# Kernel optimization log

Measured on AMD Instinct MI355X. Metric: run time of the kernel, lower is better.

## Reference

```python
import jax, jax.numpy as jnp
import numpy as np
from jax.scipy.linalg import cholesky, solve_triangular, cho_solve

N, M, D = 16384, 2048, 8
VAR, LS = 1.0, 0.5      # RBF kernel hyperparameters (same for kernel_f and kernel_g)
JITTER = 1e-6
BATCH_RATE = 1.0
HALF_LOG_2PI = 0.5 * float(np.log(2.0 * np.pi))


def rbf(x1, x2):
    # K[i,j] = VAR * exp(-||x1_i - x2_j||^2 / (2 LS^2))
    d2 = (jnp.sum(x1 * x1, 1)[:, None] + jnp.sum(x2 * x2, 1)[None, :]
          - 2.0 * (x1 @ x2.T))
    return VAR * jnp.exp(-0.5 * d2 / (LS * LS))


def setup_inputs() -> dict:
    key = jax.random.key(0)
    ks = jax.random.split(key, 7)
    x = jax.random.normal(ks[0], (N, D), dtype=jnp.float32)
    y = jax.random.normal(ks[1], (N, 1), dtype=jnp.float32)
    z = 2.0 * jax.random.uniform(ks[2], (M, D), dtype=jnp.float32) - 1.0  # inducing inputs in [-1,1]^D
    q_m_f = 0.5 * jax.random.normal(ks[3], (M, 1), dtype=jnp.float32)
    q_m_g = 0.5 * jax.random.normal(ks[4], (M, 1), dtype=jnp.float32)
    # Cholesky-like params: identity plus small strictly-lower noise -> PD covariance
    q_L_f = jnp.eye(M, dtype=jnp.float32) + 0.01 * jnp.tril(
        jax.random.normal(ks[5], (M, M), dtype=jnp.float32), -1)
    q_L_g = jnp.eye(M, dtype=jnp.float32) + 0.01 * jnp.tril(
        jax.random.normal(ks[6], (M, M), dtype=jnp.float32), -1)
    return {"x": x, "y": y, "z": z, "q_m_f": q_m_f, "q_L_f": q_L_f,
            "q_m_g": q_m_g, "q_L_g": q_L_g}


def _gp_marginals_and_kl(x, z, q_m, q_L_raw):
    """Marginal posterior mean/var at x and KL(q(u)||p(u)) for one sparse GP."""
    L_S = jnp.tril(q_L_raw)                     # [M,M]
    Kuu = rbf(z, z) + JITTER * jnp.eye(M, dtype=x.dtype)
    Lk = cholesky(Kuu, lower=True)
    Kfu = rbf(x, z)                             # [N,M]
    # A = Kfu @ Kuu^{-1}
    A = cho_solve((Lk, True), Kfu.T).T          # [N,M]
    m = (A @ q_m)[:, 0]                         # [N]
    # diag(Kff + A (S - Kuu) A^T) = diag(Kff) + diag(A S A^T) - diag(Kfu A^T)
    S = L_S @ L_S.T
    diag_Kff = jnp.full((x.shape[0],), VAR, dtype=x.dtype)
    v = diag_Kff + jnp.sum((A @ S) * A, axis=1) - jnp.sum(A * Kfu, axis=1)
    # KL(N(q_m, S) || N(0, Kuu))
    alpha = solve_triangular(Lk, q_m, lower=True)       # Kuu^{-1/2} m
    W = solve_triangular(Lk, L_S, lower=True)           # Kuu^{-1/2} L_S
    logdet_K = 2.0 * jnp.sum(jnp.log(jnp.diag(Lk)))
    logdet_S = 2.0 * jnp.sum(jnp.log(jnp.abs(jnp.diag(L_S))))
    kl = 0.5 * (jnp.sum(W * W) + jnp.sum(alpha * alpha)
                - jnp.asarray(M, x.dtype) + logdet_K - logdet_S)
    return m, v, kl


def reference(x, y, z, q_m_f, q_L_f, q_m_g, q_L_g):
    m_f, v_f, kl_f = _gp_marginals_and_kl(x, z, q_m_f, q_L_f)
    m_g, v_g, kl_g = _gp_marginals_and_kl(x, z, q_m_g, q_L_g)
    yv = y[:, 0]
    # HetGaussian variational expectation (Saul et al. 2016):
    # E_q[log N(y | f, exp(g))] per point
    expectation = (-HALF_LOG_2PI - 0.5 * m_g
                   - 0.5 * ((yv - m_f) ** 2 + v_f) * jnp.exp(-m_g + 0.5 * v_g))
    elbo = BATCH_RATE * jnp.sum(expectation) - (kl_f + kl_g)
    return -elbo
```

## Files before the change

### kernel.cpp

```cpp
#include <hip/hip_runtime.h>
#include <math.h>

#define NN 16384
#define MM 2048
#define DD 8
#define NB 32
#define GRIDN 512
#define SZB ((size_t)16777216)

constexpr float HLOG2PI = 0.91893853320467274178f;

using short8  = __attribute__((ext_vector_type(8))) short;
using float4v = __attribute__((ext_vector_type(4))) float;

__device__ __forceinline__ float4v f4zero(){ float4v v; v[0]=0.f; v[1]=0.f; v[2]=0.f; v[3]=0.f; return v; }

__device__ __forceinline__ void bfsplit(float v, short& h, short& lo){
  unsigned b = __float_as_uint(v);
  h = (short)(b >> 16);
  float hf = __uint_as_float(b & 0xFFFF0000u);
  lo = (short)(__float_as_uint(v - hf) >> 16);
}
__device__ __forceinline__ float bf2f(short s){
  return __uint_as_float(((unsigned)(unsigned short)s) << 16);
}
__device__ __forceinline__ float4v mfma3(short8 ah, short8 al, short8 bh, short8 bl, float4v c){
  c = __builtin_amdgcn_mfma_f32_16x16x32_bf16(ah, bh, c, 0, 0, 0);
  c = __builtin_amdgcn_mfma_f32_16x16x32_bf16(ah, bl, c, 0, 0, 0);
  c = __builtin_amdgcn_mfma_f32_16x16x32_bf16(al, bh, c, 0, 0, 0);
  return c;
}

__device__ __forceinline__ void gbar0(int* cnt, int* flag, int& gen){
  __syncthreads();
  if (threadIdx.x == 0){
    ++gen;
    __builtin_amdgcn_fence(__ATOMIC_RELEASE, "agent");
    int old = __hip_atomic_fetch_add(cnt, 1, __ATOMIC_RELAXED, __HIP_MEMORY_SCOPE_AGENT);
    if (old == gen*GRIDN - 1){
      __builtin_amdgcn_fence(__ATOMIC_ACQ_REL, "agent");
      __hip_atomic_store(flag, gen, __ATOMIC_RELAXED, __HIP_MEMORY_SCOPE_AGENT);
    } else {
      while (__hip_atomic_load(flag, __ATOMIC_RELAXED, __HIP_MEMORY_SCOPE_AGENT) < gen)
        __builtin_amdgcn_s_sleep(8);
    }
    __builtin_amdgcn_fence(__ATOMIC_ACQUIRE, "agent");
  }
  __syncthreads();
}

__device__ __forceinline__ void gbar_h(int* bar, int xcc, int myN, int nxcd, int& gen){
  __syncthreads();
  if (threadIdx.x == 0){
    ++gen;
    int* lcnt  = bar + xcc*32;
    int* lflag = bar + 512 + xcc*32;
    int* gcnt  = bar + 1024;
    int* gflag = bar + 1056;
    int old = __hip_atomic_fetch_add(lcnt, 1, __ATOMIC_RELAXED, __HIP_MEMORY_SCOPE_AGENT);
    if (old == gen*myN - 1){
      __builtin_amdgcn_fence(__ATOMIC_RELEASE, "agent");
      int g = __hip_atomic_fetch_add(gcnt, 1, __ATOMIC_RELAXED, __HIP_MEMORY_SCOPE_AGENT);
      if (g == gen*nxcd - 1){
        __hip_atomic_store(gflag, gen, __ATOMIC_RELAXED, __HIP_MEMORY_SCOPE_AGENT);
      } else {
        while (__hip_atomic_load(gflag, __ATOMIC_RELAXED, __HIP_MEMORY_SCOPE_AGENT) < gen)
          __builtin_amdgcn_s_sleep(8);
      }
      __builtin_amdgcn_fence(__ATOMIC_ACQUIRE, "agent");
      __hip_atomic_store(lflag, gen, __ATOMIC_RELAXED, __HIP_MEMORY_SCOPE_AGENT);
    } else {
      while (__hip_atomic_load(lflag, __ATOMIC_RELAXED, __HIP_MEMORY_SCOPE_AGENT) < gen)
        __builtin_amdgcn_s_sleep(8);
      __builtin_amdgcn_fence(__ATOMIC_ACQUIRE, "agent");
    }
  }
  __syncthreads();
}

__device__ __forceinline__ float block_reduce(float v, float* scratch){
  int lane = threadIdx.x & 63;
  int w    = threadIdx.x >> 6;
  #pragma unroll
  for (int off=32; off; off>>=1) v += __shfl_down(v, off, 64);
  __syncthreads();
  if (lane==0) scratch[w] = v;
  __syncthreads();
  float r = 0.f;
  if (threadIdx.x < 4) r = scratch[threadIdx.x];
  if (w==0){ r += __shfl_down(r, 2, 64); r += __shfl_down(r, 1, 64); }
  return r;
}

__device__ __forceinline__ void stage64(float (*S)[68], const float* __restrict__ g, int ld, int t){
  #pragma unroll
  for (int p=t; p<1024; p+=256)
    *(float4*)&S[p>>4][(p&15)*4] = *(const float4*)&g[(size_t)(p>>4)*ld + (p&15)*4];
}
__device__ __forceinline__ void tile_gemm_step(float acc[4][4], const float (*As)[68], const float (*Bs)[68], int tx, int ty){
  for (int k=0;k<64;++k){
    float ar[4], bc4[4];
    #pragma unroll
    for (int u=0;u<4;++u){ ar[u]=As[ty*4+u][k]; bc4[u]=Bs[k][tx*4+u]; }
    #pragma unroll
    for (int u=0;u<4;++u)
      #pragma unroll
      for (int v=0;v<4;++v) acc[u][v] += ar[u]*bc4[v];
  }
}
__device__ __forceinline__ void tile_syrk_step(float acc[4][4], const float (*P)[68], const float (*Q)[68], int tx, int ty){
  for (int k=0;k<64;++k){
    float pr[4], qc[4];
    #pragma unroll
    for (int u=0;u<4;++u){ pr[u]=P[ty*4+u][k]; qc[u]=Q[tx*4+u][k]; }
    #pragma unroll
    for (int u=0;u<4;++u)
      #pragma unroll
      for (int v=0;v<4;++v) acc[u][v] += pr[u]*qc[v];
  }
}

__device__ __forceinline__ void factor64_reg(const float (*S)[68],
    float* __restrict__ lkd, float* __restrict__ sdg_, int d, int t){
  if (t < 64){
    float xr[64];
    #pragma unroll
    for (int c4=0;c4<16;++c4) *(float4*)&xr[c4*4] = *(const float4*)&S[t][c4*4];
    float myrp = 1.f;
    #pragma unroll
    for (int j=0;j<64;++j){
      float ajj = __shfl(xr[j], j, 64);
      float piv = sqrtf(fmaxf(ajj, 1e-20f));
      float rp  = 1.f/piv;
      float val = xr[j]*rp;
      if (t==j){ xr[j] = piv; myrp = rp; }
      else if (t>j) xr[j] = val;
      else val = 0.f;
      #pragma unroll
      for (int c=j+1;c<64;++c){
        float vc = __shfl(val, c, 64);
        if (c<=t) xr[c] -= val*vc;
      }
    }
    #pragma unroll
    for (int c=0;c<64;++c) if (c>t) xr[c] = 0.f;
    #pragma unroll
    for (int c4=0;c4<16;++c4)
      *(float4*)&lkd[d*4096 + t*64 + c4*4] = *(float4*)&xr[c4*4];
    sdg_[d*64 + t] = myrp;
  }
}

__global__ __launch_bounds__(256, 2) void factor_coop(
    const float* __restrict__ z,
    const float* __restrict__ qlf, const float* __restrict__ qlg,
    const float* __restrict__ qmf, const float* __restrict__ qmg,
    float* __restrict__ kuu, float* __restrict__ linv,
    float* __restrict__ wf, float* __restrict__ wg,
    float* __restrict__ af, float* __restrict__ ag,
    float* __restrict__ ptmp, float* __restrict__ lkdiag,
    float* __restrict__ sdg, float* __restrict__ ltri, int* __restrict__ bar)
{
  __shared__ float As[64][68];
  __shared__ float Bs[64][68];
  __shared__ float Cs[64][68];
  __shared__ float sd[64];
  __shared__ int binfo[2];
  const int bid = blockIdx.x, t = threadIdx.x;
  const int tx = t & 15, ty = t >> 4;

  int xcc_r;
  asm volatile("s_getreg_b32 %0, hwreg(HW_REG_XCC_ID)" : "=s"(xcc_r));
  const int xcc = xcc_r & 15;
  if (t == 0)
    __hip_atomic_fetch_add(bar + 1152 + xcc*32, 1, __ATOMIC_RELAXED, __HIP_MEMORY_SCOPE_AGENT);
  int gen0 = 0;
  gbar0(bar + 1088, bar + 1120, gen0);
  if (t == 0){
    int myN = __hip_atomic_load(bar + 1152 + xcc*32, __ATOMIC_RELAXED, __HIP_MEMORY_SCOPE_AGENT);
    int nx = 0;
    for (int i=0;i<16;++i)
      nx += (__hip_atomic_load(bar + 1152 + i*32, __ATOMIC_RELAXED, __HIP_MEMORY_SCOPE_AGENT) > 0);
    binfo[0] = myN; binfo[1] = nx;
  }
  __syncthreads();
  const int myN = binfo[0], nxcd = binfo[1];
  int gen = 0;

  if (bid == 0){
    for (int p=t; p<128; p+=256){ int i=p>>1, h=p&1;
      *(float4*)&As[i][h*4] = *(const float4*)&z[(size_t)i*DD + h*4]; }
    __syncthreads();
    float kv[4][4];
    #pragma unroll
    for (int u=0;u<4;++u)
      #pragma unroll
      for (int v=0;v<4;++v){
        float d2=0.f;
        #pragma unroll
        for (int d=0;d<8;++d){ float df=As[ty*4+u][d]-As[tx*4+v][d]; d2+=df*df; }
        kv[u][v] = __expf(-2.f*d2) + ((ty*4+u)==(tx*4+v) ? 1e-6f : 0.f);
      }
    __syncthreads();
    #pragma unroll
    for (int u=0;u<4;++u)
      #pragma unroll
      for (int v=0;v<4;++v) As[ty*4+u][tx*4+v] = kv[u][v];
    __syncthreads();
    factor64_reg(As, lkdiag, sdg, 0, t);
  } else {
    for (int idx=bid; idx<528; idx+=GRIDN-1){
      int r=0; while ((r+1)*(r+2)/2 <= idx) ++r;
      int c = idx - r*(r+1)/2;
      __syncthreads();
      for (int p=t; p<128; p+=256){ int i=p>>1, h=p&1;
        *(float4*)&As[i][h*4] = *(const float4*)&z[(size_t)(r*64+i)*DD + h*4];
        *(float4*)&Bs[i][h*4] = *(const float4*)&z[(size_t)(c*64+i)*DD + h*4]; }
      __syncthreads();
      #pragma unroll
      for (int u=0;u<4;++u){
        float4 o;
        float* ov = (float*)&o;
        #pragma unroll
        for (int v=0;v<4;++v){
          float d2=0.f;
          #pragma unroll
          for (int d=0;d<8;++d){ float df=As[ty*4+u][d]-Bs[tx*4+v][d]; d2+=df*df; }
          float val = __expf(-2.f*d2);
          if (r*64+ty*4+u == c*64+tx*4+v) val += 1e-6f;
          ov[v] = val;
        }
        *(float4*)&kuu[(size_t)(r*64+ty*4+u)*MM + c*64 + tx*4] = o;
      }
    }
  }
  gbar_h(bar, xcc, myN, nxcd, gen);

  for (int kb=0; kb<31; ++kb){
    int T = NB-1 - kb;
    int ntiles = T*(T+1)/2;
    if (bid < ntiles){
      stage64(Cs, lkdiag + kb*4096, 64, t);
      if (t < 64) sd[t] = sdg[kb*64 + t];
    }
    for (int idx=bid; idx<ntiles; idx+=GRIDN){
      int r=0; while ((r+1)*(r+2)/2 <= idx) ++r;
      int c = idx - r*(r+1)/2;
      int bi = kb+1+r, bc = kb+1+c;
      __syncthreads();
      stage64(As, kuu + (size_t)(bi*64)*MM + kb*64, MM, t);
      if (bc != bi) stage64(Bs, kuu + (size_t)(bc*64)*MM + kb*64, MM, t);
      __syncthreads();
      {
        int w = t>>6, l = t&63;
        if (w==0 || (w==1 && bc!=bi)){
          float (*S)[68] = (w==0)? As : Bs;
          float xr[64];
          #pragma unroll
          for (int c4=0;c4<16;++c4) *(float4*)&xr[c4*4] = *(const float4*)&S[l][c4*4];
          #pragma unroll
          for (int j=0;j<64;++j){
            float xj = xr[j]*sd[j];
            xr[j] = xj;
            #pragma unroll
            for (int cc=j+1;cc<64;++cc) xr[cc] -= xj*Cs[cc][j];
          }
          #pragma unroll
          for (int c4=0;c4<16;++c4) *(float4*)&S[l][c4*4] = *(float4*)&xr[c4*4];
        }
      }
      __syncthreads();
      if (bc == kb+1){
        for (int p=t;p<1024;p+=256)
          *(float4*)&ltri[(size_t)(bi*64+(p>>4))*MM + kb*64 + (p&15)*4] =
              *(float4*)&As[p>>4][(p&15)*4];
      }
      float acc[4][4] = {};
      tile_syrk_step(acc, As, (bc==bi)? As : Bs, tx, ty);
      if (bi==kb+1 && bc==kb+1){
        __syncthreads();
        #pragma unroll
        for (int u=0;u<4;++u)
          #pragma unroll
          for (int v=0;v<4;++v) Bs[ty*4+u][tx*4+v] = acc[u][v];
        __syncthreads();
        for (int p=t;p<1024;p+=256){
          int i=p>>4, c4=p&15;
          float4 kv = *(const float4*)&kuu[(size_t)(bi*64+i)*MM + bi*64 + c4*4];
          float4 bv = *(float4*)&Bs[i][c4*4];
          float4 o; o.x=kv.x-bv.x; o.y=kv.y-bv.y; o.z=kv.z-bv.z; o.w=kv.w-bv.w;
          *(float4*)&As[i][c4*4] = o;
        }
        __syncthreads();
        factor64_reg(As, lkdiag, sdg, kb+1, t);
      } else {
        #pragma unroll
        for (int u=0;u<4;++u){
          float4* dst = (float4*)&kuu[(size_t)(bi*64+ty*4+u)*MM + bc*64 + tx*4];
          float4 o = *dst;
          o.x-=acc[u][0]; o.y-=acc[u][1]; o.z-=acc[u][2]; o.w-=acc[u][3];
          *dst = o;
        }
      }
    }
    gbar_h(bar, xcc, myN, nxcd, gen);
  }

  if (bid < NB){
    stage64(As, lkdiag + bid*4096, 64, t);
    __syncthreads();
    if (t < 64){
      for (int j=0;j<64;++j){
        float s = (j==t)?1.f:0.f;
        for (int k=t;k<j;++k) s -= As[j][k]*Bs[k][t];
        Bs[j][t] = (j>=t)? s/As[j][j] : 0.f;
      }
    }
    __syncthreads();
    for (int p=t;p<1024;p+=256){ int i=p>>4, c4=p&15;
      *(float4*)&linv[(size_t)(bid*64+i)*MM + bid*64 + c4*4] = *(float4*)&Bs[i][c4*4]; }
  }
  gbar_h(bar, xcc, myN, nxcd, gen);

  for (int idx=bid; idx<16; idx+=GRIDN){
    int m = idx;
    __syncthreads();
    stage64(As, ltri + (size_t)((2*m+1)*64)*MM + (2*m)*64, MM, t);
    stage64(Bs, linv + (size_t)((2*m)*64)*MM   + (2*m)*64, MM, t);
    __syncthreads();
    float acc[4][4]={};
    tile_gemm_step(acc, As, Bs, tx, ty);
    __syncthreads();
    #pragma unroll
    for (int u=0;u<4;++u)
      #pragma unroll
      for (int v=0;v<4;++v) Bs[ty*4+u][tx*4+v] = acc[u][v];
    stage64(As, linv + (size_t)((2*m+1)*64)*MM + (2*m+1)*64, MM, t);
    __syncthreads();
    float o[4][4]={};
    tile_gemm_step(o, As, Bs, tx, ty);
    #pragma unroll
    for (int u=0;u<4;++u)
      *(float4*)&linv[(size_t)((2*m+1)*64+ty*4+u)*MM + (2*m)*64 + tx*4] =
          make_float4(-o[u][0],-o[u][1],-o[u][2],-o[u][3]);
  }
  gbar_h(bar, xcc, myN, nxcd, gen);

  for (int m=bid; m<8; m+=GRIDN){
    float* pm = ptmp + (size_t)m*128*128;
    for (int ti=0; ti<2; ++ti)
      for (int tj=0; tj<2; ++tj){
        int rb = m*4 + 2 + ti, cb0 = m*4;
        float acc[4][4]={};
        for (int k=tj; k<2; ++k){
          __syncthreads();
          stage64(As, ltri + (size_t)(rb*64)*MM + (cb0+k)*64, MM, t);
          stage64(Bs, linv + (size_t)((cb0+k)*64)*MM + (cb0+tj)*64, MM, t);
          __syncthreads();
          tile_gemm_step(acc, As, Bs, tx, ty);
        }
        #pragma unroll
        for (int u=0;u<4;++u)
          *(float4*)&pm[(size_t)(ti*64+ty*4+u)*128 + tj*64 + tx*4] =
              make_float4(acc[u][0],acc[u][1],acc[u][2],acc[u][3]);
      }
    for (int ti=0; ti<2; ++ti)
      for (int tj=0; tj<2; ++tj){
        int rb = m*4 + 2 + ti;
        float acc[4][4]={};
        for (int k=0; k<=ti; ++k){
          __syncthreads();
          stage64(As, linv + (size_t)(rb*64)*MM + (m*4+2+k)*64, MM, t);
          stage64(Bs, pm + (size_t)(k*64)*128 + tj*64, 128, t);
          __syncthreads();
          tile_gemm_step(acc, As, Bs, tx, ty);
        }
        #pragma unroll
        for (int u=0;u<4;++u)
          *(float4*)&linv[(size_t)(rb*64+ty*4+u)*MM + (m*4+tj)*64 + tx*4] =
              make_float4(-acc[u][0],-acc[u][1],-acc[u][2],-acc[u][3]);
      }
  }
  gbar_h(bar, xcc, myN, nxcd, gen);

  for (int s=2; s<5; ++s){
    int nb = 1<<s, mc = 16>>s, b = 64<<s;
    float* pmb = ptmp + (s==2 ? 131072 : (s==3 ? 393216 : 917504));
    int tiles = mc*nb*nb;
    for (int idx=bid; idx<tiles; idx+=GRIDN){
      int m = idx/(nb*nb), r2 = idx%(nb*nb);
      int ti = r2/nb, tj = r2%nb;
      int rb = m*2*nb + nb + ti, cb0 = m*2*nb;
      float acc[4][4]={};
      for (int k=tj; k<nb; ++k){
        __syncthreads();
        stage64(As, ltri + (size_t)(rb*64)*MM + (cb0+k)*64, MM, t);
        stage64(Bs, linv + (size_t)((cb0+k)*64)*MM + (cb0+tj)*64, MM, t);
        __syncthreads();
        tile_gemm_step(acc, As, Bs, tx, ty);
      }
      float* pm = pmb + (size_t)m*b*b;
      #pragma unroll
      for (int u=0;u<4;++u)
        *(float4*)&pm[(size_t)(ti*64+ty*4+u)*b + tj*64 + tx*4] =
            make_float4(acc[u][0],acc[u][1],acc[u][2],acc[u][3]);
    }
    gbar_h(bar, xcc, myN, nxcd, gen);
    for (int idx=bid; idx<tiles; idx+=GRIDN){
      int m = idx/(nb*nb), r2 = idx%(nb*nb);
      int ti = r2/nb, tj = r2%nb;
      int rb = m*2*nb + nb + ti;
      const float* pm = pmb + (size_t)m*b*b;
      float acc[4][4]={};
      for (int k=0; k<=ti; ++k){
        __syncthreads();
        stage64(As, linv + (size_t)(rb*64)*MM + (m*2*nb+nb+k)*64, MM, t);
        stage64(Bs, pm + (size_t)(k*64)*b + tj*64, b, t);
        __syncthreads();
        tile_gemm_step(acc, As, Bs, tx, ty);
      }
      #pragma unroll
      for (int u=0;u<4;++u)
        *(float4*)&linv[(size_t)(rb*64+ty*4+u)*MM + (m*2*nb+tj)*64 + tx*4] =
            make_float4(-acc[u][0],-acc[u][1],-acc[u][2],-acc[u][3]);
    }
    gbar_h(bar, xcc, myN, nxcd, gen);
  }

  for (int idx=bid; idx<2*528; idx+=GRIDN){
    int gp = idx/528, rem = idx%528;
    int bi=0; while ((bi+1)*(bi+2)/2 <= rem) ++bi;
    int bj = rem - bi*(bi+1)/2;
    const float* ql = gp ? qlg : qlf;
    float* w        = gp ? wg  : wf;
    float acc[4][4]={};
    for (int bk=bj; bk<=bi; ++bk){
      __syncthreads();
      stage64(As, linv + (size_t)(bi*64)*MM + bk*64, MM, t);
      stage64(Bs, ql   + (size_t)(bk*64)*MM + bj*64, MM, t);
      __syncthreads();
      if (bk==bj){
        for (int p=t;p<4096;p+=256){ int i=p>>6, c=p&63; if (i<c) Bs[i][c]=0.f; }
        __syncthreads();
      }
      tile_gemm_step(acc, As, Bs, tx, ty);
    }
    #pragma unroll
    for (int u=0;u<4;++u)
      *(float4*)&w[(size_t)(bi*64+ty*4+u)*MM + bj*64 + tx*4] =
          make_float4(acc[u][0],acc[u][1],acc[u][2],acc[u][3]);
  }
  {
    int gw = bid*4 + (t>>6), l = t&63;
    for (int job=gw; job<4096; job+=GRIDN*4){
      int gp = job>>11, r = job&2047;
      const float* qm = gp ? qmg : qmf;
      float s=0.f;
      for (int c=l; c<=r; c+=64) s += linv[(size_t)r*MM+c]*qm[c];
      #pragma unroll
      for (int off=32; off; off>>=1) s += __shfl_down(s, off, 64);
      if (l==0) (gp ? ag : af)[r] = s;
    }
  }
}


__global__ __launch_bounds__(256) void zfrag_kernel(const float* __restrict__ z,
    short* __restrict__ zfh, short* __restrict__ zfl, float* __restrict__ zn2){
  int zr = blockIdx.x*256 + threadIdx.x;
  float v[DD]; float s = 0.f;
  #pragma unroll
  for (int d=0; d<DD; ++d){ v[d] = z[zr*DD + d]; s += v[d]*v[d]; }
  zn2[zr] = s;
  size_t base = (size_t)(zr >> 4)*512 + (zr & 15)*32;
  #pragma unroll
  for (int k=0; k<32; ++k){
    short h = 0, lo = 0;
    if (k < DD) bfsplit(v[k], h, lo);
    zfh[base + k] = h; zfl[base + k] = lo;
  }
}

__global__ __launch_bounds__(256) void red_small(const float* __restrict__ lkd,
    const float* __restrict__ qlf, const float* __restrict__ qlg,
    const float* __restrict__ af, const float* __restrict__ ag,
    float* __restrict__ scal){
  __shared__ float scratch[4];
  float ldk=0, ldf=0, ldg=0, a2f=0, a2g=0;
  for (int i=threadIdx.x;i<MM;i+=256){
    int kb = i>>6, r = i&63;
    ldk += __logf(lkd[kb*4096 + r*64 + r]);
    ldf += __logf(fabsf(qlf[(size_t)i*MM+i]));
    ldg += __logf(fabsf(qlg[(size_t)i*MM+i]));
    float v = af[i]; a2f += v*v;
    v = ag[i];       a2g += v*v;
  }
  float r;
  r = block_reduce(ldk, scratch); if (threadIdx.x==0) scal[0] = 2.f*r;
  r = block_reduce(ldf, scratch); if (threadIdx.x==0) scal[1] = 2.f*r;
  r = block_reduce(ldg, scratch); if (threadIdx.x==0) scal[2] = 2.f*r;
  r = block_reduce(a2f, scratch); if (threadIdx.x==0) scal[3] = r;
  r = block_reduce(a2g, scratch); if (threadIdx.x==0) scal[4] = r;
}

__global__ __launch_bounds__(256) void redw_kernel(const float* __restrict__ wf,
    const float* __restrict__ wg, float* __restrict__ scal){
  __shared__ float scratch[4];
  size_t start  = (size_t)blockIdx.x*256 + threadIdx.x;
  size_t stride = (size_t)gridDim.x*256;
  float sf=0, sg=0;
  for (size_t p=start;p<(size_t)MM*MM;p+=stride){
    float v=wf[p]; sf += v*v;
    v=wg[p];       sg += v*v;
  }
  float r = block_reduce(sf, scratch);
  if (threadIdx.x==0) atomicAdd(&scal[5], r);
  r = block_reduce(sg, scratch);
  if (threadIdx.x==0) atomicAdd(&scal[6], r);
}

__global__ void kl_kernel(const float* __restrict__ scal, float* __restrict__ out){
  float klf = 0.5f*(scal[5] + scal[3] - (float)MM + scal[0] - scal[1]);
  float klg = 0.5f*(scal[6] + scal[4] - (float)MM + scal[0] - scal[2]);
  out[0] += klf + klg;
}

__global__ __launch_bounds__(256) void split_rowmajor(const float* __restrict__ src,
    short* __restrict__ dh, short* __restrict__ dl){
  int p = blockIdx.x*256 + threadIdx.x;
  int chunk = p >> 9, wi = p & 511;
  int mo = chunk >> 6, ko = chunk & 63;
  int row = mo*16 + (wi >> 5), col = ko*32 + (wi & 31);
  float v = src[(size_t)row*MM + col];
  short h, lo; bfsplit(v, h, lo);
  dh[p] = h; dl[p] = lo;
}

__global__ __launch_bounds__(256) void split_transpose(const float* __restrict__ src,
    short* __restrict__ dh, short* __restrict__ dl){
  __shared__ float tile[32][33];
  int t = threadIdx.x;
  int mb = blockIdx.x, kb = blockIdx.y;
  #pragma unroll
  for (int k=0;k<4;++k){
    int idx = t + k*256;
    int lr = idx >> 5, lc = idx & 31;
    tile[lr][lc] = src[(size_t)(kb*32+lr)*MM + mb*32 + lc];
  }
  __syncthreads();
  #pragma unroll
  for (int e=0;e<4;++e){
    int p = t*4 + e;
    int c = p >> 9, wi = p & 511;
    int i = (wi >> 5) & 15, kk = wi & 31;
    float v = tile[kk][c*16 + i];
    short h, lo; bfsplit(v, h, lo);
    size_t gp = ((size_t)(mb*2 + c)*64 + kb)*512 + wi;
    dh[gp] = h; dl[gp] = lo;
  }
}

__global__ __launch_bounds__(256, 2) void tt_mfma(
    const float* __restrict__ x, const float* __restrict__ zn2,
    const short* __restrict__ zfh, const short* __restrict__ zfl,
    const short* __restrict__ lvh, const short* __restrict__ lvl,
    short* __restrict__ tth, short* __restrict__ ttl){
  __shared__ __align__(16) short lAh[8192], lAl[8192], lBh[8192], lBl[8192];
  int t = threadIdx.x;
  int l = t & 63, w = t >> 6;
  int istrip = blockIdx.x, bj2 = blockIdx.y;
  int li = l & 15, q = l >> 4;
  int lofs = li*32 + q*8;
  int wn4 = (w>>1)*4, wm4 = (w&1)*4;

  short8 xh[2], xl[2];
  float xn2v[8];
  {
    float xn2t[2];
    #pragma unroll
    for (int tn=0; tn<2; ++tn){
      int n = istrip*128 + w*32 + tn*16 + li;
      const float4* xp = (const float4*)(x + (size_t)n*DD);
      float4 p0 = xp[0], p1 = xp[1];
      float v[8] = {p0.x,p0.y,p0.z,p0.w,p1.x,p1.y,p1.z,p1.w};
      float s = 0.f;
      #pragma unroll
      for (int d=0; d<8; ++d) s += v[d]*v[d];
      xn2t[tn] = s;
      short8 hh, ll;
      #pragma unroll
      for (int j=0; j<8; ++j){
        short h=0, lo=0;
        if (q==0) bfsplit(v[j], h, lo);
        hh[j]=h; ll[j]=lo;
      }
      xh[tn]=hh; xl[tn]=ll;
    }
    #pragma unroll
    for (int tn=0; tn<2; ++tn)
      #pragma unroll
      for (int r=0; r<4; ++r)
        xn2v[tn*4+r] = __shfl(xn2t[tn], q*4 + r, 64);
  }

  float4v acc[4][4];
  #pragma unroll
  for (int i=0;i<4;++i)
    #pragma unroll
    for (int j=0;j<4;++j) acc[i][j] = f4zero();

  int nkt = 2*bj2 + 2;
  for (int bk=0; bk<nkt; ++bk){
    __syncthreads();
    {
      short8 zh[4], zl[4];
      float zt2[4];
      #pragma unroll
      for (int tz=0; tz<4; ++tz){
        size_t zo = (size_t)(bk*4 + tz)*512 + lofs;
        zh[tz] = *(const short8*)(zfh + zo);
        zl[tz] = *(const short8*)(zfl + zo);
        zt2[tz] = zn2[bk*64 + tz*16 + li];
      }
      #pragma unroll
      for (int tn=0; tn<2; ++tn){
        #pragma unroll
        for (int tz=0; tz<4; ++tz){
          float4v s4 = mfma3(xh[tn], xl[tn], zh[tz], zl[tz], f4zero());
          #pragma unroll
          for (int r=0; r<4; ++r){
            float e = __expf(4.f*s4[r] - 2.f*(xn2v[tn*4+r] + zt2[tz]));
            short h, lo; bfsplit(e, h, lo);
            int pos = ((w*2+tn)*2 + (tz>>1))*512 + (q*4+r)*32 + (tz&1)*16 + li;
            lAh[pos] = h; lAl[pos] = lo;
          }
        }
      }
    }
    #pragma unroll
    for (int c4 = t; c4 < 1024; c4 += 256){
      int ch = c4 >> 6, wdi = c4 & 63;
      size_t g = ((size_t)(bj2*8 + (ch>>1))*64 + (size_t)(bk*2 + (ch&1)))*64 + wdi;
      ((uint4*)lBh)[c4] = ((const uint4*)lvh)[g];
      ((uint4*)lBl)[c4] = ((const uint4*)lvl)[g];
    }
    __syncthreads();
    #pragma unroll
    for (int s=0; s<2; ++s){
      short8 ah[4], al[4], bh[4], bl[4];
      #pragma unroll
      for (int tn=0; tn<4; ++tn){
        int off = ((wn4+tn)*2 + s)*512 + lofs;
        ah[tn] = *(const short8*)&lAh[off];
        al[tn] = *(const short8*)&lAl[off];
      }
      #pragma unroll
      for (int tm=0; tm<4; ++tm){
        int off = ((wm4+tm)*2 + s)*512 + lofs;
        bh[tm] = *(const short8*)&lBh[off];
        bl[tm] = *(const short8*)&lBl[off];
      }
      #pragma unroll
      for (int tn=0; tn<4; ++tn)
        #pragma unroll
        for (int tm=0; tm<4; ++tm)
          acc[tn][tm] = mfma3(ah[tn], al[tn], bh[tm], bl[tm], acc[tn][tm]);
    }
  }
  #pragma unroll
  for (int tn=0; tn<4; ++tn){
    int no_g = istrip*8 + wn4 + tn;
    #pragma unroll
    for (int tm=0; tm<4; ++tm){
      int mo_g = bj2*4 + (w&1)*2 + (tm>>1);
      size_t cb = ((size_t)no_g*64 + mo_g)*512;
      #pragma unroll
      for (int r=0; r<4; ++r){
        short h, lo; bfsplit(acc[tn][tm][r], h, lo);
        size_t pos = cb + (q*4+r)*32 + (tm&1)*16 + li;
        tth[pos] = h; ttl[pos] = lo;
      }
    }
  }
}

__global__ __launch_bounds__(256) void lin_v2(const short* __restrict__ tth,
    const short* __restrict__ ttl, const float* __restrict__ af, const float* __restrict__ ag,
    float* __restrict__ t2, float* __restrict__ lf, float* __restrict__ lg){
  int t = threadIdx.x;
  int w = t >> 6, l = t & 63;
  int n = blockIdx.x*4 + w;
  int g = l >> 2, j = l & 3;
  float s2=0.f, sf=0.f, sg=0.f;
  #pragma unroll
  for (int it=0; it<4; ++it){
    int ck = g + it*16;
    size_t off = ((size_t)(n>>4)*64 + ck)*512 + (n&15)*32 + j*8;
    short8 h8 = *(const short8*)(tth + off);
    short8 l8 = *(const short8*)(ttl + off);
    int m0 = ck*32 + j*8;
    float4 a0 = *(const float4*)(af + m0), a1 = *(const float4*)(af + m0 + 4);
    float4 g0 = *(const float4*)(ag + m0), g1 = *(const float4*)(ag + m0 + 4);
    float av[8] = {a0.x,a0.y,a0.z,a0.w,a1.x,a1.y,a1.z,a1.w};
    float gv[8] = {g0.x,g0.y,g0.z,g0.w,g1.x,g1.y,g1.z,g1.w};
    #pragma unroll
    for (int e=0; e<8; ++e){
      float tv = bf2f(h8[e]) + bf2f(l8[e]);
      s2 += tv*tv; sf += tv*av[e]; sg += tv*gv[e];
    }
  }
  #pragma unroll
  for (int off=32; off; off>>=1){
    s2 += __shfl_down(s2, off, 64);
    sf += __shfl_down(sf, off, 64);
    sg += __shfl_down(sg, off, 64);
  }
  if (l==0){ t2[n] = s2; lf[n] = sf; lg[n] = sg; }
}

__global__ __launch_bounds__(256, 2) void quad_mfma(
    const short* __restrict__ tth, const short* __restrict__ ttl,
    const short* __restrict__ wfh, const short* __restrict__ wfl,
    const short* __restrict__ wgh, const short* __restrict__ wgl,
    float* __restrict__ vfq, float* __restrict__ vgq){
  __shared__ __align__(16) short lAh[8192], lAl[8192], lBh[8192], lBl[8192];
  int t = threadIdx.x, l = t & 63, w = t >> 6;
  int istrip = blockIdx.x, bj2 = blockIdx.y;
  const short* gbh = blockIdx.z ? wgh : wfh;
  const short* gbl = blockIdx.z ? wgl : wfl;
  float* vq = blockIdx.z ? vgq : vfq;
  int li = l & 15, q = l >> 4;
  int lofs = li*32 + q*8;
  int wn4 = (w>>1)*4, wm4 = (w&1)*4;

  float4v acc[4][4];
  #pragma unroll
  for (int i=0;i<4;++i)
    #pragma unroll
    for (int j=0;j<4;++j) acc[i][j] = f4zero();

  for (int bk=2*bj2; bk<32; ++bk){
    __syncthreads();
    #pragma unroll
    for (int c4 = t; c4 < 1024; c4 += 256){
      int ch = c4 >> 6, wdi = c4 & 63;
      size_t ga = ((size_t)(istrip*8 + (ch>>1))*64 + (size_t)(bk*2 + (ch&1)))*64 + wdi;
      ((uint4*)lAh)[c4] = ((const uint4*)tth)[ga];
      ((uint4*)lAl)[c4] = ((const uint4*)ttl)[ga];
      size_t gb = ((size_t)(bj2*8 + (ch>>1))*64 + (size_t)(bk*2 + (ch&1)))*64 + wdi;
      ((uint4*)lBh)[c4] = ((const uint4*)gbh)[gb];
      ((uint4*)lBl)[c4] = ((const uint4*)gbl)[gb];
    }
    __syncthreads();
    #pragma unroll
    for (int s=0; s<2; ++s){
      short8 ah[4], al[4], bh[4], bl[4];
      #pragma unroll
      for (int tn=0; tn<4; ++tn){
        int off = ((wn4+tn)*2 + s)*512 + lofs;
        ah[tn] = *(const short8*)&lAh[off];
        al[tn] = *(const short8*)&lAl[off];
      }
      #pragma unroll
      for (int tm=0; tm<4; ++tm){
        int off = ((wm4+tm)*2 + s)*512 + lofs;
        bh[tm] = *(const short8*)&lBh[off];
        bl[tm] = *(const short8*)&lBl[off];
      }
      #pragma unroll
      for (int tn=0; tn<4; ++tn)
        #pragma unroll
        for (int tm=0; tm<4; ++tm)
          acc[tn][tm] = mfma3(ah[tn], al[tn], bh[tm], bl[tm], acc[tn][tm]);
    }
  }
  float rs[16];
  #pragma unroll
  for (int tn=0; tn<4; ++tn)
    #pragma unroll
    for (int r=0; r<4; ++r){
      float s = 0.f;
      #pragma unroll
      for (int tm=0; tm<4; ++tm){ float v = acc[tn][tm][r]; s += v*v; }
      rs[tn*4+r] = s;
    }
  #pragma unroll
  for (int off=8; off; off>>=1)
    #pragma unroll
    for (int k=0; k<16; ++k) rs[k] += __shfl_down(rs[k], off, 16);
  if (li == 0){
    #pragma unroll
    for (int tn=0; tn<4; ++tn)
      #pragma unroll
      for (int r=0; r<4; ++r){
        int n = istrip*128 + (w>>1)*64 + tn*16 + q*4 + r;
        atomicAdd(&vq[n], rs[tn*4+r]);
      }
  }
}

__global__ __launch_bounds__(256) void final_kernel(const float* __restrict__ y,
    const float* __restrict__ t2, const float* __restrict__ lf, const float* __restrict__ lg,
    const float* __restrict__ vfq, const float* __restrict__ vgq, float* __restrict__ out){
  __shared__ float scratch[4];
  int i = blockIdx.x*256 + threadIdx.x;
  float mf = lf[i], mg = lg[i];
  float vf = 1.f + vfq[i] - t2[i];
  float vg = 1.f + vgq[i] - t2[i];
  float dy = y[i] - mf;
  float e = -HLOG2PI - 0.5f*mg - 0.5f*(dy*dy + vf)*__expf(-mg + 0.5f*vg);
  float r = block_reduce(e, scratch);
  if (threadIdx.x==0) atomicAdd(out, -r);
}

extern "C" void kernel_launch(void* const* d_in, const int* in_sizes, int n_in,
                              void* d_out, int out_size, void* d_ws, size_t ws_size,
                              hipStream_t stream){
  (void)in_sizes; (void)n_in; (void)out_size; (void)ws_size;
  const float* x   = (const float*)d_in[0];
  const float* y   = (const float*)d_in[1];
  const float* z   = (const float*)d_in[2];
  const float* qmf = (const float*)d_in[3];
  const float* qlf = (const float*)d_in[4];
  const float* qmg = (const float*)d_in[5];
  const float* qlg = (const float*)d_in[6];
  float* out = (float*)d_out;
  char* Bw = (char*)d_ws;

  float* kuu  = (float*)Bw;
  float* linv = (float*)(Bw + SZB);
  float* wf   = (float*)(Bw + 2*SZB);
  float* wg   = (float*)(Bw + 3*SZB);
  short* lvh  = (short*)Bw;
  short* lvl  = (short*)(Bw + SZB/2);
  short* wfh  = (short*)(Bw + SZB);
  short* wfl  = (short*)(Bw + SZB + SZB/2);
  short* wgh  = (short*)(Bw + 2*SZB);
  short* wgl  = (short*)(Bw + 2*SZB + SZB/2);
  short* tth  = (short*)(Bw + 3*SZB);
  short* ttl  = (short*)(Bw + 3*SZB + (size_t)NN*MM*2);
  float* ltri   = (float*)(Bw + 4*SZB);
  float* ptmp   = (float*)(Bw + 5*SZB);
  float* lkdiag = (float*)(Bw + 5*SZB + (size_t)8388608);
  float* sdg    = (float*)(Bw + 5*SZB + (size_t)8388608 + (size_t)524288);
  float* sm   = (float*)(Bw + 3*SZB + (size_t)NN*MM*4);
  float* af = sm;          float* ag = af + MM;
  float* t2 = ag + MM;     float* lf = t2 + NN;   float* lg = lf + NN;
  float* vfq = lg + NN;    float* vgq = vfq + NN; float* scal = vgq + NN;
  int*   bar = (int*)(scal + 64);
  float* zn2 = scal + 64 + 2048;
  short* zfh = (short*)(zn2 + MM);
  short* zfl = zfh + MM*32;

  hipMemsetAsync(out, 0, sizeof(float), stream);
  hipMemsetAsync(vfq, 0, (size_t)(2*NN + 64 + 2048)*sizeof(float), stream);
  hipMemsetAsync(wf,  0, 2*SZB, stream);
  hipMemsetAsync(linv,0, SZB,   stream);

  zfrag_kernel<<<MM/256, 256, 0, stream>>>(z, zfh, zfl, zn2);

  factor_coop<<<GRIDN, 256, 0, stream>>>(z, qlf, qlg, qmf, qmg,
                                         kuu, linv, wf, wg, af, ag,
                                         ptmp, lkdiag, sdg, ltri, bar);

  red_small<<<1, 256, 0, stream>>>(lkdiag, qlf, qlg, af, ag, scal);
  redw_kernel<<<512, 256, 0, stream>>>(wf, wg, scal);
  kl_kernel<<<1, 1, 0, stream>>>(scal, out);

  split_rowmajor<<<MM*MM/256, 256, 0, stream>>>(linv, lvh, lvl);
  split_transpose<<<dim3(MM/32, MM/32), 256, 0, stream>>>(wf, wfh, wfl);
  split_transpose<<<dim3(MM/32, MM/32), 256, 0, stream>>>(wg, wgh, wgl);

  tt_mfma<<<dim3(NN/128, MM/128), 256, 0, stream>>>(x, zn2, zfh, zfl, lvh, lvl, tth, ttl);
  lin_v2<<<NN/4, 256, 0, stream>>>(tth, ttl, af, ag, t2, lf, lg);
  quad_mfma<<<dim3(NN/128, MM/128, 2), 256, 0, stream>>>(tth, ttl, wfh, wfl, wgh, wgl, vfq, vgq);
  final_kernel<<<NN/256, 256, 0, stream>>>(y, t2, lf, lg, vfq, vgq, out);
}
```

Measured before the change: 4.600 ms.

## Replace bulk-synchronous blocked Cholesky with dataflow tile scheduling using ready flags

The 31 grid-wide barriers of the right-looking blocked Cholesky are replaced by a left-looking, tile-granular dataflow scheme. Each block computes one lower-triangular tile, spin-waits on per-tile ready flags for its dependencies, and accumulates its SYRK/GEMM updates from ltri before factoring or triangular-solving. Flags and tile data use relaxed agent-scope atomics. The grid is also halved to 256 blocks. The intent is to cut barrier latency along the serial critical path. In exchange, flag-ordering correctness rests on relaxed atomics without explicit fences, and the left-looking loop re-reads ltri panels more often.

```diff
diff --git a/kernel.cpp b/kernel.cpp
--- a/kernel.cpp
+++ b/kernel.cpp
@@ -5,7 +5,7 @@
 #define MM 2048
 #define DD 8
 #define NB 32
-#define GRIDN 512
+#define GRIDN 256
 #define SZB ((size_t)16777216)
 
 constexpr float HLOG2PI = 0.91893853320467274178f;
@@ -29,6 +29,24 @@
   c = __builtin_amdgcn_mfma_f32_16x16x32_bf16(ah, bl, c, 0, 0, 0);
   c = __builtin_amdgcn_mfma_f32_16x16x32_bf16(al, bh, c, 0, 0, 0);
   return c;
+}
+
+union U8 { unsigned long long u; float f[2]; };
+__device__ __forceinline__ unsigned long long ald8(const float* p){
+  return __hip_atomic_load((const unsigned long long*)p, __ATOMIC_RELAXED, __HIP_MEMORY_SCOPE_AGENT);
+}
+__device__ __forceinline__ void ast8(float* p, unsigned long long v){
+  __hip_atomic_store((unsigned long long*)p, v, __ATOMIC_RELAXED, __HIP_MEMORY_SCOPE_AGENT);
+}
+__device__ __forceinline__ void ast8f(float* p, float a, float b){
+  U8 u; u.f[0]=a; u.f[1]=b;
+  __hip_atomic_store((unsigned long long*)p, u.u, __ATOMIC_RELAXED, __HIP_MEMORY_SCOPE_AGENT);
+}
+__device__ __forceinline__ void ast4(float* p, float v){
+  __hip_atomic_store(p, v, __ATOMIC_RELAXED, __HIP_MEMORY_SCOPE_AGENT);
+}
+__device__ __forceinline__ float ald4f(const float* p){
+  return __hip_atomic_load(p, __ATOMIC_RELAXED, __HIP_MEMORY_SCOPE_AGENT);
 }
 
 __device__ __forceinline__ void gbar0(int* cnt, int* flag, int& gen){
@@ -97,6 +115,16 @@
   for (int p=t; p<1024; p+=256)
     *(float4*)&S[p>>4][(p&15)*4] = *(const float4*)&g[(size_t)(p>>4)*ld + (p&15)*4];
 }
+__device__ __forceinline__ void stage64_a(float (*S)[68], const float* __restrict__ g, int ld, int t){
+  #pragma unroll
+  for (int p=t; p<1024; p+=256){
+    int r = p>>4, c0 = (p&15)*4;
+    const float* src = &g[(size_t)r*ld + c0];
+    unsigned long long v0 = ald8(src), v1 = ald8(src+2);
+    *(unsigned long long*)&S[r][c0]   = v0;
+    *(unsigned long long*)&S[r][c0+2] = v1;
+  }
+}
 __device__ __forceinline__ void tile_gemm_step(float acc[4][4], const float (*As)[68], const float (*Bs)[68], int tx, int ty){
   for (int k=0;k<64;++k){
     float ar[4], bc4[4];
@@ -120,7 +148,7 @@
   }
 }
 
-__device__ __forceinline__ void factor64_reg(const float (*S)[68],
+__device__ __forceinline__ void factor64_sc1(const float (*S)[68],
     float* __restrict__ lkd, float* __restrict__ sdg_, int d, int t){
   if (t < 64){
     float xr[64];
@@ -145,13 +173,13 @@
     #pragma unroll
     for (int c=0;c<64;++c) if (c>t) xr[c] = 0.f;
     #pragma unroll
-    for (int c4=0;c4<16;++c4)
-      *(float4*)&lkd[d*4096 + t*64 + c4*4] = *(float4*)&xr[c4*4];
-    sdg_[d*64 + t] = myrp;
-  }
-}
-
-__global__ __launch_bounds__(256, 2) void factor_coop(
+    for (int c2=0;c2<32;++c2)
+      ast8f(&lkd[d*4096 + t*64 + c2*2], xr[c2*2], xr[c2*2+1]);
+    ast4(&sdg_[d*64 + t], myrp);
+  }
+}
+
+__global__ __launch_bounds__(256) void factor_coop(
     const float* __restrict__ z,
     const float* __restrict__ qlf, const float* __restrict__ qlg,
     const float* __restrict__ qmf, const float* __restrict__ qmg,
@@ -186,125 +214,106 @@
   __syncthreads();
   const int myN = binfo[0], nxcd = binfo[1];
   int gen = 0;
-
-  if (bid == 0){
+  int* rdy = bar + 2048;
+
+  for (int idx=bid; idx<528; idx+=GRIDN){
+    int r=0; while ((r+1)*(r+2)/2 <= idx) ++r;
+    int c = idx - r*(r+1)/2;
+    __syncthreads();
     for (int p=t; p<128; p+=256){ int i=p>>1, h=p&1;
-      *(float4*)&As[i][h*4] = *(const float4*)&z[(size_t)i*DD + h*4]; }
-    __syncthreads();
-    float kv[4][4];
-    #pragma unroll
-    for (int u=0;u<4;++u)
+      *(float4*)&As[i][h*4] = *(const float4*)&z[(size_t)(r*64+i)*DD + h*4];
+      *(float4*)&Bs[i][h*4] = *(const float4*)&z[(size_t)(c*64+i)*DD + h*4]; }
+    __syncthreads();
+    #pragma unroll
+    for (int u=0;u<4;++u){
+      float4 o;
+      float* ov = (float*)&o;
       #pragma unroll
       for (int v=0;v<4;++v){
         float d2=0.f;
         #pragma unroll
-        for (int d=0;d<8;++d){ float df=As[ty*4+u][d]-As[tx*4+v][d]; d2+=df*df; }
-        kv[u][v] = __expf(-2.f*d2) + ((ty*4+u)==(tx*4+v) ? 1e-6f : 0.f);
-      }
-    __syncthreads();
-    #pragma unroll
-    for (int u=0;u<4;++u)
-      #pragma unroll
-      for (int v=0;v<4;++v) As[ty*4+u][tx*4+v] = kv[u][v];
-    __syncthreads();
-    factor64_reg(As, lkdiag, sdg, 0, t);
-  } else {
-    for (int idx=bid; idx<528; idx+=GRIDN-1){
-      int r=0; while ((r+1)*(r+2)/2 <= idx) ++r;
-      int c = idx - r*(r+1)/2;
-      __syncthreads();
-      for (int p=t; p<128; p+=256){ int i=p>>1, h=p&1;
-        *(float4*)&As[i][h*4] = *(const float4*)&z[(size_t)(r*64+i)*DD + h*4];
-        *(float4*)&Bs[i][h*4] = *(const float4*)&z[(size_t)(c*64+i)*DD + h*4]; }
-      __syncthreads();
-      #pragma unroll
-      for (int u=0;u<4;++u){
-        float4 o;
-        float* ov = (float*)&o;
+        for (int d=0;d<8;++d){ float df=As[ty*4+u][d]-Bs[tx*4+v][d]; d2+=df*df; }
+        float val = __expf(-2.f*d2);
+        if (r*64+ty*4+u == c*64+tx*4+v) val += 1e-6f;
+        ov[v] = val;
+      }
+      *(float4*)&kuu[(size_t)(r*64+ty*4+u)*MM + c*64 + tx*4] = o;
+    }
+  }
+  gbar_h(bar, xcc, myN, nxcd, gen);
+
+  for (int p = bid; p < 528; p += GRIDN){
+    int j = 0;
+    while (32*(j+1) - ((j+1)*j)/2 <= p) ++j;
+    int i = j + (p - (32*j - (j*(j-1))/2));
+    float acc[4][4] = {};
+    for (int k = 0; k < j; ++k){
+      if (t == 0){
+        while (__hip_atomic_load(rdy + i*32 + k, __ATOMIC_RELAXED, __HIP_MEMORY_SCOPE_AGENT) == 0)
+          __builtin_amdgcn_s_sleep(2);
+        if (i != j)
+          while (__hip_atomic_load(rdy + j*32 + k, __ATOMIC_RELAXED, __HIP_MEMORY_SCOPE_AGENT) == 0)
+            __builtin_amdgcn_s_sleep(2);
+      }
+      __syncthreads();
+      stage64_a(As, ltri + (size_t)(i*64)*MM + k*64, MM, t);
+      if (i != j) stage64_a(Bs, ltri + (size_t)(j*64)*MM + k*64, MM, t);
+      __syncthreads();
+      tile_syrk_step(acc, As, (i==j)? As : Bs, tx, ty);
+      __syncthreads();
+    }
+    #pragma unroll
+    for (int u=0;u<4;++u){
+      float4 kvv = *(const float4*)&kuu[(size_t)(i*64+ty*4+u)*MM + j*64 + tx*4];
+      As[ty*4+u][tx*4  ] = kvv.x - acc[u][0];
+      As[ty*4+u][tx*4+1] = kvv.y - acc[u][1];
+      As[ty*4+u][tx*4+2] = kvv.z - acc[u][2];
+      As[ty*4+u][tx*4+3] = kvv.w - acc[u][3];
+    }
+    __syncthreads();
+    if (i == j){
+      factor64_sc1(As, lkdiag, sdg, j, t);
+      __syncthreads();
+      if (t == 0)
+        __hip_atomic_store(rdy + j*32 + j, 1, __ATOMIC_RELAXED, __HIP_MEMORY_SCOPE_AGENT);
+    } else {
+      if (t == 0){
+        while (__hip_atomic_load(rdy + j*32 + j, __ATOMIC_RELAXED, __HIP_MEMORY_SCOPE_AGENT) == 0)
+          __builtin_amdgcn_s_sleep(2);
+      }
+      __syncthreads();
+      stage64_a(Cs, lkdiag + j*4096, 64, t);
+      if (t < 64) sd[t] = ald4f(sdg + j*64 + t);
+      __syncthreads();
+      if (t < 64){
+        int l = t;
+        float xr[64];
         #pragma unroll
-        for (int v=0;v<4;++v){
-          float d2=0.f;
+        for (int c4=0;c4<16;++c4) *(float4*)&xr[c4*4] = *(const float4*)&As[l][c4*4];
+        #pragma unroll
+        for (int jj=0;jj<64;++jj){
+          float xj = xr[jj]*sd[jj];
+          xr[jj] = xj;
           #pragma unroll
-          for (int d=0;d<8;++d){ float df=As[ty*4+u][d]-Bs[tx*4+v][d]; d2+=df*df; }
-          float val = __expf(-2.f*d2);
-          if (r*64+ty*4+u == c*64+tx*4+v) val += 1e-6f;
-          ov[v] = val;
+          for (int cc=jj+1;cc<64;++cc) xr[cc] -= xj*Cs[cc][jj];
         }
-        *(float4*)&kuu[(size_t)(r*64+ty*4+u)*MM + c*64 + tx*4] = o;
-      }
-    }
+        #pragma unroll
+        for (int c4=0;c4<16;++c4) *(float4*)&As[l][c4*4] = *(float4*)&xr[c4*4];
+      }
+      __syncthreads();
+      for (int q=t; q<1024; q+=256){
+        int rr=q>>4, c0=(q&15)*4;
+        float* dst = &ltri[(size_t)(i*64+rr)*MM + j*64 + c0];
+        ast8(dst,   *(const unsigned long long*)&As[rr][c0]);
+        ast8(dst+2, *(const unsigned long long*)&As[rr][c0+2]);
+      }
+      __syncthreads();
+      if (t == 0)
+        __hip_atomic_store(rdy + i*32 + j, 1, __ATOMIC_RELAXED, __HIP_MEMORY_SCOPE_AGENT);
+    }
+    __syncthreads();
   }
   gbar_h(bar, xcc, myN, nxcd, gen);
-
-  for (int kb=0; kb<31; ++kb){
-    int T = NB-1 - kb;
-    int ntiles = T*(T+1)/2;
-    if (bid < ntiles){
-      stage64(Cs, lkdiag + kb*4096, 64, t);
-      if (t < 64) sd[t] = sdg[kb*64 + t];
-    }
-    for (int idx=bid; idx<ntiles; idx+=GRIDN){
-      int r=0; while ((r+1)*(r+2)/2 <= idx) ++r;
-      int c = idx - r*(r+1)/2;
-      int bi = kb+1+r, bc = kb+1+c;
-      __syncthreads();
-      stage64(As, kuu + (size_t)(bi*64)*MM + kb*64, MM, t);
-      if (bc != bi) stage64(Bs, kuu + (size_t)(bc*64)*MM + kb*64, MM, t);
-      __syncthreads();
-      {
-        int w = t>>6, l = t&63;
-        if (w==0 || (w==1 && bc!=bi)){
-          float (*S)[68] = (w==0)? As : Bs;
-          float xr[64];
-          #pragma unroll
-          for (int c4=0;c4<16;++c4) *(float4*)&xr[c4*4] = *(const float4*)&S[l][c4*4];
-          #pragma unroll
-          for (int j=0;j<64;++j){
-            float xj = xr[j]*sd[j];
-            xr[j] = xj;
-            #pragma unroll
-            for (int cc=j+1;cc<64;++cc) xr[cc] -= xj*Cs[cc][j];
-          }
-          #pragma unroll
-          for (int c4=0;c4<16;++c4) *(float4*)&S[l][c4*4] = *(float4*)&xr[c4*4];
-        }
-      }
-      __syncthreads();
-      if (bc == kb+1){
-        for (int p=t;p<1024;p+=256)
-          *(float4*)&ltri[(size_t)(bi*64+(p>>4))*MM + kb*64 + (p&15)*4] =
-              *(float4*)&As[p>>4][(p&15)*4];
-      }
-      float acc[4][4] = {};
-      tile_syrk_step(acc, As, (bc==bi)? As : Bs, tx, ty);
-      if (bi==kb+1 && bc==kb+1){
-        __syncthreads();
-        #pragma unroll
-        for (int u=0;u<4;++u)
-          #pragma unroll
-          for (int v=0;v<4;++v) Bs[ty*4+u][tx*4+v] = acc[u][v];
-        __syncthreads();
-        for (int p=t;p<1024;p+=256){
-          int i=p>>4, c4=p&15;
-          float4 kv = *(const float4*)&kuu[(size_t)(bi*64+i)*MM + bi*64 + c4*4];
-          float4 bv = *(float4*)&Bs[i][c4*4];
-          float4 o; o.x=kv.x-bv.x; o.y=kv.y-bv.y; o.z=kv.z-bv.z; o.w=kv.w-bv.w;
-          *(float4*)&As[i][c4*4] = o;
-        }
-        __syncthreads();
-        factor64_reg(As, lkdiag, sdg, kb+1, t);
-      } else {
-        #pragma unroll
-        for (int u=0;u<4;++u){
-          float4* dst = (float4*)&kuu[(size_t)(bi*64+ty*4+u)*MM + bc*64 + tx*4];
-          float4 o = *dst;
-          o.x-=acc[u][0]; o.y-=acc[u][1]; o.z-=acc[u][2]; o.w-=acc[u][3];
-          *dst = o;
-        }
-      }
-    }
-    gbar_h(bar, xcc, myN, nxcd, gen);
-  }
 
   if (bid < NB){
     stage64(As, lkdiag + bid*4096, 64, t);
@@ -848,12 +857,12 @@
   float* t2 = ag + MM;     float* lf = t2 + NN;   float* lg = lf + NN;
   float* vfq = lg + NN;    float* vgq = vfq + NN; float* scal = vgq + NN;
   int*   bar = (int*)(scal + 64);
-  float* zn2 = scal + 64 + 2048;
+  float* zn2 = scal + 64 + 2048 + 1024;
   short* zfh = (short*)(zn2 + MM);
   short* zfl = zfh + MM*32;
 
   hipMemsetAsync(out, 0, sizeof(float), stream);
-  hipMemsetAsync(vfq, 0, (size_t)(2*NN + 64 + 2048)*sizeof(float), stream);
+  hipMemsetAsync(vfq, 0, (size_t)(2*NN + 64 + 2048 + 1024)*sizeof(float), stream);
   hipMemsetAsync(wf,  0, 2*SZB, stream);
   hipMemsetAsync(linv,0, SZB,   stream);
 
```

Measured after the change: 5.158 ms. 12.1% more time.
